# Kernel tuning notes

Measured on AMD Instinct MI355X. Metric: run time of the kernel, lower is better.

Reference implementation:

```python
import jax, jax.numpy as jnp
import numpy as np

DIMS, IN_DIM, OUT_DIM = 64, 128, 128
B, S = 16384, 4


def setup_inputs() -> dict:
    key = jax.random.key(0)
    k1, k2, k3, k4 = jax.random.split(key, 4)
    lookups = jax.random.randint(k1, (B,), 0, DIMS, dtype=jnp.int64)
    values = jax.random.normal(k2, (B, S, IN_DIM), dtype=jnp.float32)
    # learned parameters: per-expert weight matrices and biases
    W = jax.random.normal(k3, (DIMS, IN_DIM, OUT_DIM), dtype=jnp.float32) * 0.02
    b = jax.random.normal(k4, (DIMS, OUT_DIM), dtype=jnp.float32) * 0.02
    return {"values": values, "W": W, "b": b, "lookups": lookups}


def reference(values, W, b, lookups):
    # gather one weight matrix / bias per sample (the big intermediate)
    w = W[lookups]                      # [B, IN_DIM, OUT_DIM]
    bias = b[lookups]                   # [B, OUT_DIM]
    mapped = jnp.einsum('bsi,bio->bso', values, w) + bias[:, None, :]
    return mapped                       # activation == 'linear' (identity)
```

## Files before the change

kernel.cpp:

```cpp
#include <hip/hip_runtime.h>
#include <hip/hip_bf16.h>
#include <stdint.h>


#define NDIMS   64
#define IN_DIM  128
#define OUT_DIM 128
#define BATCH   16384
#define SEQ     4
#define NC      8
#define CHUNK   (BATCH / NC)
#define THREADS 256
#define NWAVE   4

using bf16x8 = __attribute__((ext_vector_type(8))) __bf16;
using f32x4  = __attribute__((ext_vector_type(4))) float;

static __device__ inline uint16_t bf16bits(float f) {
    __bf16 h = (__bf16)f;
    return __builtin_bit_cast(uint16_t, h);
}

static __device__ inline bf16x8 cvt8(f32x4 v0, f32x4 v1) {
    bf16x8 r;
    r[0] = (__bf16)v0[0]; r[1] = (__bf16)v0[1];
    r[2] = (__bf16)v0[2]; r[3] = (__bf16)v0[3];
    r[4] = (__bf16)v1[0]; r[5] = (__bf16)v1[1];
    r[6] = (__bf16)v1[2]; r[7] = (__bf16)v1[3];
    return r;
}

__global__ __launch_bounds__(THREADS)
void multidense_kernel(const float* __restrict__ values,
                       const float* __restrict__ W,
                       const float* __restrict__ bias,
                       const int*   __restrict__ lookups,
                       float*       __restrict__ out)
{
    __shared__ __align__(16) unsigned char w_lds[OUT_DIM * IN_DIM * 2];
    __shared__ int list[CHUNK];
    __shared__ int nm_sh;

    const int tid = threadIdx.x;
    const int e   = blockIdx.x >> 3;
    const int c   = blockIdx.x & (NC - 1);

    if (tid == 0) nm_sh = 0;
    __syncthreads();

    {
        const float* We = W + (size_t)e * IN_DIM * OUT_DIM;
        const int o   = tid & 127;
        const int ih  = tid >> 7;
        const int swz = (o & 7) << 4;
        unsigned char* wrow = &w_lds[o * 256];
        #pragma unroll 4
        for (int ii = 0; ii < 32; ++ii) {
            int i0 = ih * 2 + ii * 4;
            float f0 = We[(i0    ) * OUT_DIM + o];
            float f1 = We[(i0 + 1) * OUT_DIM + o];
            uint32_t pk = (uint32_t)bf16bits(f0) | ((uint32_t)bf16bits(f1) << 16);
            *(uint32_t*)(wrow + ((i0 * 2) ^ swz)) = pk;
        }
    }

    {
        const int cbase = c * CHUNK;
        for (int t = tid; t < CHUNK; t += THREADS) {
            if (lookups[cbase + t] == e) {
                int p = atomicAdd(&nm_sh, 1);
                list[p] = cbase + t;
            }
        }
    }
    __syncthreads();

    const int nm = nm_sh;
    if (nm == 0) return;

    const int lane = tid & 63;
    const int wid  = tid >> 6;
    const int l15  = lane & 15;
    const int l4   = lane >> 4;
    const int swzB = (l15 & 7) << 4;

    float bias_c[8];
    #pragma unroll
    for (int nf = 0; nf < 8; ++nf) bias_c[nf] = bias[e * OUT_DIM + nf * 16 + l15];

    for (int grp = wid; grp * 8 < nm; grp += NWAVE) {
        const int sbase = grp * 8;

        const float* pA[2];
        #pragma unroll
        for (int mf = 0; mf < 2; ++mf) {
            int row  = mf * 16 + l15;
            int pos  = sbase + (row >> 2);
            int posc = pos < nm ? pos : nm - 1;
            int b    = list[posc];
            pA[mf] = values + (size_t)(b * SEQ + (row & 3)) * IN_DIM + l4 * 8;
        }

        f32x4 acc[2][8];
        #pragma unroll
        for (int mf = 0; mf < 2; ++mf)
            #pragma unroll
            for (int nf = 0; nf < 8; ++nf) {
                f32x4 a; a[0] = bias_c[nf]; a[1] = bias_c[nf]; a[2] = bias_c[nf]; a[3] = bias_c[nf];
                acc[mf][nf] = a;
            }

        #pragma unroll
        for (int ks = 0; ks < 4; ++ks) {
            bf16x8 afr[2];
            #pragma unroll
            for (int mf = 0; mf < 2; ++mf) {
                f32x4 v0 = *(const f32x4*)(pA[mf] + ks * 32);
                f32x4 v1 = *(const f32x4*)(pA[mf] + ks * 32 + 4);
                afr[mf] = cvt8(v0, v1);
            }
            const int koff = (ks * 64 + l4 * 16) ^ swzB;
            #pragma unroll
            for (int nf = 0; nf < 8; ++nf) {
                const bf16x8 bfr = *(const bf16x8*)(&w_lds[(nf * 16 + l15) * 256 + koff]);
                acc[0][nf] = __builtin_amdgcn_mfma_f32_16x16x32_bf16(afr[0], bfr, acc[0][nf], 0, 0, 0);
                acc[1][nf] = __builtin_amdgcn_mfma_f32_16x16x32_bf16(afr[1], bfr, acc[1][nf], 0, 0, 0);
            }
        }

        #pragma unroll
        for (int mf = 0; mf < 2; ++mf) {
            #pragma unroll
            for (int r = 0; r < 4; ++r) {
                int row = mf * 16 + l4 * 4 + r;
                int pos = sbase + (row >> 2);
                if (pos < nm) {
                    int b = list[pos];
                    float* po = out + (size_t)(b * SEQ + (row & 3)) * OUT_DIM + l15;
                    #pragma unroll
                    for (int nf = 0; nf < 8; ++nf) po[nf * 16] = acc[mf][nf][r];
                }
            }
        }
    }
}

extern "C" void kernel_launch(void* const* d_in, const int* in_sizes, int n_in,
                              void* d_out, int out_size, void* d_ws, size_t ws_size,
                              hipStream_t stream) {
    const float* values  = (const float*)d_in[0];
    const float* W       = (const float*)d_in[1];
    const float* bias    = (const float*)d_in[2];
    const int*   lookups = (const int*)d_in[3];
    float* out = (float*)d_out;

    hipLaunchKernelGGL(multidense_kernel, dim3(NDIMS * NC), dim3(THREADS), 0, stream,
                       values, W, bias, lookups, out);
}
```

Measured before the change: 32.78 us.

## Double chunk count, shrink per-wave tile, and widen weight LDS staging

Splits each expert's batch into 16 chunks instead of 8, giving 1024 blocks. Each wave now processes 4 samples (one 16-row MFMA tile) instead of 8. The index list is stored as 16-bit values, and the block order is changed so that the blocks for different experts interleave. Weight staging writes 8-byte packed bf16 quads with a per-row rotation to spread load and store conflicts, and launch bounds request 4 blocks per CU. The aim is better occupancy and load balance for the small per-expert workloads, at the cost of twice as many redundant weight conversions per expert.

```diff
diff --git a/kernel.cpp b/kernel.cpp
--- a/kernel.cpp
+++ b/kernel.cpp
@@ -8,10 +8,11 @@
 #define OUT_DIM 128
 #define BATCH   16384
 #define SEQ     4
-#define NC      8
+#define NC      16
 #define CHUNK   (BATCH / NC)
 #define THREADS 256
 #define NWAVE   4
+#define GRP     4
 
 using bf16x8 = __attribute__((ext_vector_type(8))) __bf16;
 using f32x4  = __attribute__((ext_vector_type(4))) float;
@@ -30,7 +31,7 @@
     return r;
 }
 
-__global__ __launch_bounds__(THREADS)
+__global__ __launch_bounds__(THREADS, 4)
 void multidense_kernel(const float* __restrict__ values,
                        const float* __restrict__ W,
                        const float* __restrict__ bias,
@@ -38,38 +39,46 @@
                        float*       __restrict__ out)
 {
     __shared__ __align__(16) unsigned char w_lds[OUT_DIM * IN_DIM * 2];
-    __shared__ int list[CHUNK];
+    __shared__ unsigned short list[CHUNK];
     __shared__ int nm_sh;
 
     const int tid = threadIdx.x;
-    const int e   = blockIdx.x >> 3;
-    const int c   = blockIdx.x & (NC - 1);
+    const int e   = blockIdx.x & 63;
+    const int c   = blockIdx.x >> 6;
 
     if (tid == 0) nm_sh = 0;
     __syncthreads();
 
     {
-        const float* We = W + (size_t)e * IN_DIM * OUT_DIM;
+        const float* We = W + (size_t)e * (IN_DIM * OUT_DIM);
         const int o   = tid & 127;
         const int ih  = tid >> 7;
+        const int rot = (o >> 3) & 15;
         const int swz = (o & 7) << 4;
         unsigned char* wrow = &w_lds[o * 256];
         #pragma unroll 4
-        for (int ii = 0; ii < 32; ++ii) {
-            int i0 = ih * 2 + ii * 4;
-            float f0 = We[(i0    ) * OUT_DIM + o];
+        for (int qq = 0; qq < 16; ++qq) {
+            int q  = ih * 16 + ((qq + rot) & 15);
+            int i0 = q * 4;
+            float f0 = We[(i0 + 0) * OUT_DIM + o];
             float f1 = We[(i0 + 1) * OUT_DIM + o];
-            uint32_t pk = (uint32_t)bf16bits(f0) | ((uint32_t)bf16bits(f1) << 16);
-            *(uint32_t*)(wrow + ((i0 * 2) ^ swz)) = pk;
+            float f2 = We[(i0 + 2) * OUT_DIM + o];
+            float f3 = We[(i0 + 3) * OUT_DIM + o];
+            uint32_t lo = (uint32_t)bf16bits(f0) | ((uint32_t)bf16bits(f1) << 16);
+            uint32_t hi = (uint32_t)bf16bits(f2) | ((uint32_t)bf16bits(f3) << 16);
+            uint64_t pk = (uint64_t)lo | ((uint64_t)hi << 32);
+            *(uint64_t*)(wrow + ((i0 * 2) ^ swz)) = pk;
         }
     }
 
     {
         const int cbase = c * CHUNK;
-        for (int t = tid; t < CHUNK; t += THREADS) {
-            if (lookups[cbase + t] == e) {
+        #pragma unroll
+        for (int t = 0; t < CHUNK / THREADS; ++t) {
+            int idx = cbase + t * THREADS + tid;
+            if (lookups[idx] == e) {
                 int p = atomicAdd(&nm_sh, 1);
-                list[p] = cbase + t;
+                list[p] = (unsigned short)idx;
             }
         }
     }
@@ -88,58 +97,44 @@
     #pragma unroll
     for (int nf = 0; nf < 8; ++nf) bias_c[nf] = bias[e * OUT_DIM + nf * 16 + l15];
 
-    for (int grp = wid; grp * 8 < nm; grp += NWAVE) {
-        const int sbase = grp * 8;
+    for (int grp = wid; grp * GRP < nm; grp += NWAVE) {
+        const int sbase = grp * GRP;
 
-        const float* pA[2];
+        int pos  = sbase + (l15 >> 2);
+        int posc = pos < nm ? pos : nm - 1;
+        int b    = (int)list[posc];
+        const float* pA = values + (size_t)(b * SEQ + (l15 & 3)) * IN_DIM + l4 * 8;
+
+        f32x4 acc[8];
         #pragma unroll
-        for (int mf = 0; mf < 2; ++mf) {
-            int row  = mf * 16 + l15;
-            int pos  = sbase + (row >> 2);
-            int posc = pos < nm ? pos : nm - 1;
-            int b    = list[posc];
-            pA[mf] = values + (size_t)(b * SEQ + (row & 3)) * IN_DIM + l4 * 8;
+        for (int nf = 0; nf < 8; ++nf) {
+            f32x4 a;
+            a[0] = bias_c[nf]; a[1] = bias_c[nf]; a[2] = bias_c[nf]; a[3] = bias_c[nf];
+            acc[nf] = a;
         }
-
-        f32x4 acc[2][8];
-        #pragma unroll
-        for (int mf = 0; mf < 2; ++mf)
-            #pragma unroll
-            for (int nf = 0; nf < 8; ++nf) {
-                f32x4 a; a[0] = bias_c[nf]; a[1] = bias_c[nf]; a[2] = bias_c[nf]; a[3] = bias_c[nf];
-                acc[mf][nf] = a;
-            }
 
         #pragma unroll
         for (int ks = 0; ks < 4; ++ks) {
-            bf16x8 afr[2];
-            #pragma unroll
-            for (int mf = 0; mf < 2; ++mf) {
-                f32x4 v0 = *(const f32x4*)(pA[mf] + ks * 32);
-                f32x4 v1 = *(const f32x4*)(pA[mf] + ks * 32 + 4);
-                afr[mf] = cvt8(v0, v1);
-            }
+            f32x4 v0 = *(const f32x4*)(pA + ks * 32);
+            f32x4 v1 = *(const f32x4*)(pA + ks * 32 + 4);
+            bf16x8 afr = cvt8(v0, v1);
             const int koff = (ks * 64 + l4 * 16) ^ swzB;
             #pragma unroll
             for (int nf = 0; nf < 8; ++nf) {
                 const bf16x8 bfr = *(const bf16x8*)(&w_lds[(nf * 16 + l15) * 256 + koff]);
-                acc[0][nf] = __builtin_amdgcn_mfma_f32_16x16x32_bf16(afr[0], bfr, acc[0][nf], 0, 0, 0);
-                acc[1][nf] = __builtin_amdgcn_mfma_f32_16x16x32_bf16(afr[1], bfr, acc[1][nf], 0, 0, 0);
+                acc[nf] = __builtin_amdgcn_mfma_f32_16x16x32_bf16(afr, bfr, acc[nf], 0, 0, 0);
             }
         }
 
         #pragma unroll
-        for (int mf = 0; mf < 2; ++mf) {
-            #pragma unroll
-            for (int r = 0; r < 4; ++r) {
-                int row = mf * 16 + l4 * 4 + r;
-                int pos = sbase + (row >> 2);
-                if (pos < nm) {
-                    int b = list[pos];
-                    float* po = out + (size_t)(b * SEQ + (row & 3)) * OUT_DIM + l15;
-                    #pragma unroll
-                    for (int nf = 0; nf < 8; ++nf) po[nf * 16] = acc[mf][nf][r];
-                }
+        for (int r = 0; r < 4; ++r) {
+            int row  = l4 * 4 + r;
+            int pos2 = sbase + (row >> 2);
+            if (pos2 < nm) {
+                int b2 = (int)list[pos2];
+                float* po = out + (size_t)(b2 * SEQ + (row & 3)) * OUT_DIM + l15;
+                #pragma unroll
+                for (int nf = 0; nf < 8; ++nf) po[nf * 16] = acc[nf][r];
             }
         }
     }
```

Result: slower. 52.80 us (+61.1%).
